# Performance work log

Measured on AMD Instinct MI355X. Metric: run time of the kernel, lower is better.

## Reference

```python
import jax, jax.numpy as jnp
import numpy as np

BIT = 4
HALF = 2 ** (BIT - 1)          # 8 -> signed integer grid [-8, 7]
N_LEVELS = 2 ** BIT - 1        # 15
COUT, CIN, KH, KW = 1024, 1024, 3, 3


def _flip_pass(r, err, up_num, up_err, up_pri, dn_num, dn_err, dn_pri):
    """One SQuant flip pass over rows (groups). Greedily flips the rounding
    direction of the highest-priority elements so each row's rounding-error
    sum becomes ~0, and hands off boundary priorities for the next pass
    (reconstruction of the SQuant_func CUDA kernel)."""
    G, K = r.shape
    rows = jnp.arange(G)
    e = err.sum(-1)                                    # (G,) error budget
    nflip = jnp.round(jnp.abs(e)).astype(jnp.int32)    # flips needed per row
    is_up = e < 0                                      # under-rounded -> flip up

    pri = jnp.where(is_up[:, None], up_pri, dn_pri)
    order = jnp.argsort(-pri, axis=-1)                 # descending priority
    rank = jnp.zeros((G, K), jnp.int32).at[rows[:, None], order].set(
        jnp.broadcast_to(jnp.arange(K, dtype=jnp.int32), (G, K)))
    flip = rank < nflip[:, None]

    cand_num = jnp.where(is_up[:, None], up_num, dn_num)
    cand_err = jnp.where(is_up[:, None], up_err, dn_err)
    new_r = jnp.where(flip, cand_num, r)
    new_err = jnp.where(flip, cand_err, err)

    # ---- boundary-priority handoff for the next (channel-wise) pass ----
    ni = jnp.take_along_axis(order, jnp.clip(nflip, 0, K - 1)[:, None], axis=-1)[:, 0]      # next candidate
    li = jnp.take_along_axis(order, jnp.clip(nflip - 1, 0, K - 1)[:, None], axis=-1)[:, 0]  # last flipped
    has_next = nflip < K
    has_last = nflip > 0
    next_pri = jnp.where(has_next, pri[rows, ni], 0.0)         # flip one more element
    last_pri = jnp.where(has_last, 1.0 - pri[rows, li], 0.0)   # revert the last flip

    z = jnp.zeros_like(pri)
    new_up_pri = z.at[rows, ni].add(jnp.where(is_up, next_pri, 0.0))
    new_up_pri = new_up_pri.at[rows, li].add(jnp.where(~is_up, last_pri, 0.0))
    new_dn_pri = z.at[rows, ni].add(jnp.where(~is_up, next_pri, 0.0))
    new_dn_pri = new_dn_pri.at[rows, li].add(jnp.where(is_up, last_pri, 0.0))

    # reverting the last flipped element restores its pre-flip value/error
    up_last = is_up & has_last
    dn_last = (~is_up) & has_last
    new_dn_num = dn_num.at[rows, li].set(jnp.where(up_last, r[rows, li], dn_num[rows, li]))
    new_dn_err = dn_err.at[rows, li].set(jnp.where(up_last, err[rows, li], dn_err[rows, li]))
    new_up_num = up_num.at[rows, li].set(jnp.where(dn_last, r[rows, li], up_num[rows, li]))
    new_up_err = up_err.at[rows, li].set(jnp.where(dn_last, err[rows, li], up_err[rows, li]))
    return new_r, new_err, new_up_num, new_up_err, new_up_pri, new_dn_num, new_dn_err, new_dn_pri


def _adaptive_round(q):
    t_min, t_max = float(-HALF), float(HALF - 1)
    r = jnp.round(q)
    err = r - q
    cand_up = (err < 0) & (q < t_max)    # elements that may be rounded up instead
    cand_dn = (err > 0) & (q > t_min)    # elements that may be rounded down instead
    up_num = jnp.where(cand_up, r + 1.0, r)
    up_err = jnp.where(cand_up, err + 1.0, 0.0)
    up_pri = jnp.where(cand_up, -err, 0.0)   # |rounding error|
    dn_num = jnp.where(cand_dn, r - 1.0, r)
    dn_err = jnp.where(cand_dn, err - 1.0, 0.0)
    dn_pri = jnp.where(cand_dn, err, 0.0)

    cout, cin = q.shape[0], q.shape[1]
    k = q.size // (cout * cin)
    st = tuple(a.reshape(cout * cin, k) for a in (r, err, up_num, up_err, up_pri, dn_num, dn_err, dn_pri))
    st = _flip_pass(*st)                               # SQuant-K: per (Cout,Cin) kernel
    st = tuple(a.reshape(cout, cin * k) for a in st)
    st = _flip_pass(*st)                               # SQuant-C: per output channel
    return st[0].reshape(q.shape)


def _squant_quantize(weight):
    flat = weight.reshape(weight.shape[0], -1)
    x_max = flat.max(1)
    x_min = flat.min(1)
    scale = N_LEVELS / jnp.maximum(x_max - x_min, 1e-8)   # asymmetric per-channel
    zp = jnp.round(scale * x_min) + HALF                  # signed, integral zero point
    bshape = (-1,) + (1,) * (weight.ndim - 1)
    scale = scale.reshape(bshape)
    zp = zp.reshape(bshape)
    q = scale * weight - zp                               # linear_quantize
    q = _adaptive_round(q)
    q = jnp.clip(q, -HALF, HALF - 1)
    return (q + zp) / scale                               # linear_dequantize


def setup_inputs() -> dict:
    key = jax.random.key(0)
    weight = jax.random.normal(key, (COUT, CIN, KH, KW), dtype=jnp.float32) * 0.05
    return {"weight": weight}


def reference(weight):
    return _squant_quantize(weight)
```

## Files before the change

### kernel.cpp

```cpp
#include <hip/hip_runtime.h>

#define NROW   1024
#define ROWLEN 9216
#define NGRP   1024
#define NT     256
#define GPT    4
#define LCAP   256

__device__ __forceinline__ int bucketOf(float v) {
    int b = (int)(v * 256.0f);
    return b > 255 ? 255 : b;
}

__device__ __forceinline__ float err2_of(float wv, int enc, float scale, float zp) {
    float q = __fsub_rn(__fmul_rn(scale, wv), zp);
    float r = rintf(q);
    float err = __fsub_rn(r, q);
    if (enc > 50) return 0.0f;
    int delta = enc - __float2int_rn(r);
    return delta ? __fadd_rn(err, (float)delta) : err;
}

__device__ void replay_group(const float* wg, float scale, float zp,
                             float r[9], float err[9], float q[9],
                             int* nflip1, bool* isup1, int* li_out) {
    float pri[9];
    #pragma unroll
    for (int j = 0; j < 9; ++j) {
        float qq = __fsub_rn(__fmul_rn(scale, wg[j]), zp);
        float rr = rintf(qq);
        q[j] = qq; r[j] = rr; err[j] = __fsub_rn(rr, qq);
    }
    float e = __fadd_rn(
                __fadd_rn(__fadd_rn(__fadd_rn(err[0], err[1]), __fadd_rn(err[2], err[3])),
                          __fadd_rn(__fadd_rn(err[4], err[5]), __fadd_rn(err[6], err[7]))),
                err[8]);
    int nf0 = (int)rintf(fabsf(e));
    bool up = (e < 0.0f);
    #pragma unroll
    for (int j = 0; j < 9; ++j) {
        bool cand = up ? ((err[j] < 0.0f) && (q[j] < 7.0f))
                       : ((err[j] > 0.0f) && (q[j] > -8.0f));
        pri[j] = cand ? (up ? -err[j] : err[j]) : 0.0f;
    }
    int rank[9] = {0,0,0,0,0,0,0,0,0};
    #pragma unroll
    for (int a = 0; a < 9; ++a)
        #pragma unroll
        for (int b = a + 1; b < 9; ++b) {
            int c = (pri[a] >= pri[b]) ? 1 : 0;
            rank[b] += c; rank[a] += 1 - c;
        }
    int nf = nf0 < 9 ? nf0 : 9;
    int lip = nf - 1; if (lip < 0) lip = 0;
    int li = 0;
    #pragma unroll
    for (int j = 0; j < 9; ++j) if (rank[j] == lip) li = j;
    *nflip1 = nf0; *isup1 = up; *li_out = li;
}

__global__ __launch_bounds__(NT, 5) void squant_kernel(const float* __restrict__ w,
                                                       float* __restrict__ out) {
    __shared__ alignas(16) signed char s_r2[ROWLEN];
    __shared__ unsigned short s_upos[NGRP];
    __shared__ unsigned short s_dpos[NGRP];
    __shared__ float s_uval[NGRP];
    __shared__ float s_dval[NGRP];
    __shared__ signed char s_ucn[NGRP];
    __shared__ signed char s_dcn[NGRP];
    __shared__ float s_leaf[128];
    __shared__ int   s_hist[256];
    __shared__ float s_lv[LCAP];
    __shared__ unsigned short s_lg[LCAP];
    __shared__ float s_wred[8];
    __shared__ float s_bc[2];
    __shared__ float s_e2s;
    __shared__ int   s_seli[2];
    __shared__ int   s_lcount;

    const int row = blockIdx.x;
    const int tid = threadIdx.x;
    const int lane = tid & 63, wid = tid >> 6;
    const float* wrow = w + (size_t)row * ROWLEN;

    float vmin =  3.402823466e38f;
    float vmax = -3.402823466e38f;
    const float4* w4 = reinterpret_cast<const float4*>(wrow);
    #pragma unroll
    for (int k = 0; k < 9; ++k) {
        float4 v = w4[tid + k * NT];
        vmin = fminf(vmin, fminf(fminf(v.x, v.y), fminf(v.z, v.w)));
        vmax = fmaxf(vmax, fmaxf(fmaxf(v.x, v.y), fmaxf(v.z, v.w)));
    }
    #pragma unroll
    for (int o = 32; o > 0; o >>= 1) {
        vmin = fminf(vmin, __shfl_xor(vmin, o, 64));
        vmax = fmaxf(vmax, __shfl_xor(vmax, o, 64));
    }
    if (lane == 0) { s_wred[wid] = vmin; s_wred[4 + wid] = vmax; }
    __syncthreads();
    if (tid == 0) {
        float a = s_wred[0], b = s_wred[4];
        #pragma unroll
        for (int i = 1; i < 4; ++i) { a = fminf(a, s_wred[i]); b = fmaxf(b, s_wred[4 + i]); }
        s_bc[0] = a; s_bc[1] = b;
    }
    __syncthreads();
    const float scale = __fdiv_rn(15.0f, fmaxf(__fsub_rn(s_bc[1], s_bc[0]), 1e-8f));
    const float zp    = __fadd_rn(rintf(__fmul_rn(scale, s_bc[0])), 8.0f);

    const float4* wt4 = reinterpret_cast<const float4*>(wrow + 36 * tid);
    #pragma unroll
    for (int gi = 0; gi < GPT; ++gi) {
        const int g = tid * GPT + gi;
        const int base = g * 9;
        const int a4 = (9 * gi) >> 2;
        float4 A = wt4[a4], B = wt4[a4 + 1], C = wt4[a4 + 2];
        float f[12] = {A.x, A.y, A.z, A.w, B.x, B.y, B.z, B.w, C.x, C.y, C.z, C.w};
        float q[9], r[9], err[9], pri[9];
        #pragma unroll
        for (int j = 0; j < 9; ++j) {
            float wv = f[gi + j];
            float qq = __fsub_rn(__fmul_rn(scale, wv), zp);
            float rr = rintf(qq);
            q[j] = qq; r[j] = rr; err[j] = __fsub_rn(rr, qq);
        }
        float e = __fadd_rn(
                    __fadd_rn(__fadd_rn(__fadd_rn(err[0], err[1]), __fadd_rn(err[2], err[3])),
                              __fadd_rn(__fadd_rn(err[4], err[5]), __fadd_rn(err[6], err[7]))),
                    err[8]);
        int nflip = (int)rintf(fabsf(e));
        const bool isup = (e < 0.0f);
        #pragma unroll
        for (int j = 0; j < 9; ++j) {
            bool cand = isup ? ((err[j] < 0.0f) && (q[j] < 7.0f))
                             : ((err[j] > 0.0f) && (q[j] > -8.0f));
            pri[j] = cand ? (isup ? -err[j] : err[j]) : 0.0f;
        }
        int rank[9] = {0,0,0,0,0,0,0,0,0};
        #pragma unroll
        for (int a = 0; a < 9; ++a)
            #pragma unroll
            for (int b = a + 1; b < 9; ++b) {
                int c = (pri[a] >= pri[b]) ? 1 : 0;
                rank[b] += c; rank[a] += 1 - c;
            }
        const int nf  = nflip < 9 ? nflip : 9;
        const int nip = nf < 8 ? nf : 8;
        int lip = nf - 1; if (lip < 0) lip = 0;

        int ni = 0, li = 0;
        float pri_ni = 0.0f, pri_li = 0.0f, r_ni = 0.0f, r_li = 0.0f;
        #pragma unroll
        for (int j = 0; j < 9; ++j) {
            bool cand = pri[j] > 0.0f;
            bool flip = rank[j] < nf;
            float cnj = cand ? (isup ? r[j] + 1.0f : r[j] - 1.0f) : r[j];
            int enc = __float2int_rn(flip ? cnj : r[j]);
            if (flip && !cand) enc += 100;
            s_r2[base + j] = (signed char)enc;
            if (rank[j] == nip) { ni = j; pri_ni = pri[j]; r_ni = r[j]; }
            if (rank[j] == lip) { li = j; pri_li = pri[j]; r_li = r[j]; }
        }
        const bool has_next = (nflip < 9);
        const bool has_last = (nflip > 0);
        const float next_pri = has_next ? pri_ni : 0.0f;
        const float last_pri = has_last ? __fsub_rn(1.0f, pri_li) : 0.0f;
        signed char ncv = (signed char)__float2int_rn(
            (pri_ni > 0.0f) ? (isup ? r_ni + 1.0f : r_ni - 1.0f) : r_ni);
        signed char lcv = (signed char)__float2int_rn(r_li);
        if (isup) {
            s_upos[g] = (unsigned short)(base + ni); s_uval[g] = next_pri; s_ucn[g] = ncv;
            s_dpos[g] = (unsigned short)(base + li); s_dval[g] = last_pri; s_dcn[g] = lcv;
        } else {
            s_dpos[g] = (unsigned short)(base + ni); s_dval[g] = next_pri; s_dcn[g] = ncv;
            s_upos[g] = (unsigned short)(base + li); s_uval[g] = last_pri; s_ucn[g] = lcv;
        }
    }
    __syncthreads();

    {
        const int l = tid >> 1, h = tid & 1;
        float a0, a1, a2, a3;
        #pragma unroll
        for (int i = 0; i < 9; ++i) {
            const int off = 72 * l + 8 * i + 4 * h;
            float4 v = *reinterpret_cast<const float4*>(wrow + off);
            int e4 = *reinterpret_cast<const int*>(s_r2 + off);
            float e0 = err2_of(v.x, (int)(signed char)(e4 & 0xff),         scale, zp);
            float e1 = err2_of(v.y, (int)(signed char)((e4 >> 8) & 0xff),  scale, zp);
            float e2v= err2_of(v.z, (int)(signed char)((e4 >> 16) & 0xff), scale, zp);
            float e3 = err2_of(v.w, (int)(signed char)((e4 >> 24) & 0xff), scale, zp);
            if (i == 0) { a0 = e0; a1 = e1; a2 = e2v; a3 = e3; }
            else {
                a0 = __fadd_rn(a0, e0); a1 = __fadd_rn(a1, e1);
                a2 = __fadd_rn(a2, e2v); a3 = __fadd_rn(a3, e3);
            }
        }
        float t = __fadd_rn(__fadd_rn(a0, a1), __fadd_rn(a2, a3));
        float o = __shfl_xor(t, 1, 64);
        if (h == 0) s_leaf[l] = __fadd_rn(t, o);
        s_hist[tid] = 0;
        if (tid == 0) s_lcount = 0;
    }
    __syncthreads();
    if (tid < 64) {
        float v = __fadd_rn(s_leaf[2 * tid], s_leaf[2 * tid + 1]);
        #pragma unroll
        for (int o = 1; o < 64; o <<= 1) {
            float u = __shfl_xor(v, o, 64);
            v = __fadd_rn(v, u);
        }
        if (tid == 0) s_e2s = v;
    }
    __syncthreads();

    const float e2     = s_e2s;
    const int   nflip2 = (int)rintf(fabsf(e2));
    const bool  isup2  = (e2 < 0.0f);
    const float* val = isup2 ? s_uval : s_dval;
    const unsigned short* pos = isup2 ? s_upos : s_dpos;
    const signed char* cnv = isup2 ? s_ucn : s_dcn;

    int   gg[4]; float vv[4]; int bb[4];
    #pragma unroll
    for (int m = 0; m < 4; ++m) {
        gg[m] = tid + m * NT;
        vv[m] = val[gg[m]];
        bb[m] = (vv[m] > 0.0f) ? bucketOf(vv[m]) : -1;
        if (bb[m] >= 0) atomicAdd(&s_hist[bb[m]], 1);
    }
    __syncthreads();
    if (tid < 64) {
        int b0 = s_hist[4*tid], b1 = s_hist[4*tid+1], b2 = s_hist[4*tid+2], b3 = s_hist[4*tid+3];
        int s3 = b3, s2 = b2 + s3, s1 = b1 + s2, s0 = b0 + s1;
        int suf = s0;
        #pragma unroll
        for (int off = 1; off < 64; off <<= 1) {
            int o = __shfl_down(suf, off, 64);
            if (tid + off < 64) suf += o;
        }
        int above = suf - s0;
        s_hist[4*tid]   = s0 + above;
        s_hist[4*tid+1] = s1 + above;
        s_hist[4*tid+2] = s2 + above;
        s_hist[4*tid+3] = s3 + above;
    }
    __syncthreads();
    const int npos = s_hist[0];

    if (nflip2 > 0 && nflip2 <= npos) {
        {
            int Tb  = s_hist[tid];
            int Tb1 = (tid < 255) ? s_hist[tid + 1] : 0;
            if (Tb >= nflip2 && Tb1 < nflip2) { s_seli[0] = tid; s_seli[1] = nflip2 - Tb1; }
        }
        __syncthreads();
        const int B = s_seli[0], m = s_seli[1];
        #pragma unroll
        for (int mm = 0; mm < 4; ++mm) {
            if (bb[mm] > B) s_r2[pos[gg[mm]]] = cnv[gg[mm]];
            else if (bb[mm] == B) {
                int ix = atomicAdd(&s_lcount, 1);
                if (ix < LCAP) { s_lv[ix] = vv[mm]; s_lg[ix] = (unsigned short)gg[mm]; }
            }
        }
        __syncthreads();
        const int L = s_lcount;
        if (L <= LCAP) {
            #pragma unroll
            for (int mm = 0; mm < 4; ++mm) {
                if (bb[mm] != B) continue;
                int rk = 0;
                for (int l = 0; l < L; ++l) {
                    float lv = s_lv[l]; int lg = s_lg[l];
                    rk += (int)((lv > vv[mm]) || ((lv == vv[mm]) && (lg < gg[mm])));
                }
                if (rk < m) s_r2[pos[gg[mm]]] = cnv[gg[mm]];
            }
        } else {
            #pragma unroll
            for (int mm = 0; mm < 4; ++mm) {
                if (bb[mm] != B) continue;
                int rk = 0;
                for (int j = 0; j < NGRP; ++j) {
                    float vj = val[j];
                    if (vj > 0.0f && bucketOf(vj) == B)
                        rk += (int)((vj > vv[mm]) || ((vj == vv[mm]) && (j < gg[mm])));
                }
                if (rk < m) s_r2[pos[gg[mm]]] = cnv[gg[mm]];
            }
        }
    } else if (nflip2 > npos) {
        #pragma unroll
        for (int mm = 0; mm < 4; ++mm)
            if (bb[mm] >= 0) s_r2[pos[gg[mm]]] = cnv[gg[mm]];
        __syncthreads();
        if (tid == 0) {
            int c = 0; const int extra = nflip2 - npos;
            for (int g = 0; g < NGRP && c < extra; ++g) {
                float r[9], err[9], q[9]; int nf1; bool up1; int li;
                replay_group(wrow + 9 * g, scale, zp, r, err, q, &nf1, &up1, &li);
                for (int j = 0; j < 9 && c < extra; ++j) {
                    int p = 9 * g + j;
                    if (val[g] > 0.0f && pos[g] == p) continue;
                    float cnp;
                    if (isup2) { bool cu = (err[j] < 0.0f) && (q[j] < 7.0f);
                                 cnp = cu ? r[j] + 1.0f : r[j]; }
                    else       { bool cd = (err[j] > 0.0f) && (q[j] > -8.0f);
                                 cnp = cd ? r[j] - 1.0f : r[j]; }
                    if (nf1 > 0 && j == li && (up1 != isup2)) cnp = r[j];
                    s_r2[p] = (signed char)__float2int_rn(cnp);
                    ++c;
                }
            }
        }
    }
    __syncthreads();

    const int* r2i = reinterpret_cast<const int*>(s_r2);
    float4* o4 = reinterpret_cast<float4*>(out + (size_t)row * ROWLEN);
    #pragma unroll
    for (int k = 0; k < 9; ++k) {
        int i = tid + k * NT;
        int word = r2i[i];
        float4 o;
        #pragma unroll
        for (int c = 0; c < 4; ++c) {
            int v = (int)(signed char)((word >> (8 * c)) & 0xff);
            if (v > 50) v -= 100;
            v = v < -8 ? -8 : (v > 7 ? 7 : v);
            float f = __fdiv_rn(__fadd_rn((float)v, zp), scale);
            if (c == 0) o.x = f; else if (c == 1) o.y = f; else if (c == 2) o.z = f; else o.w = f;
        }
        o4[i] = o;
    }
}

extern "C" void kernel_launch(void* const* d_in, const int* in_sizes, int n_in,
                              void* d_out, int out_size, void* d_ws, size_t ws_size,
                              hipStream_t stream) {
    const float* w = (const float*)d_in[0];
    float* out = (float*)d_out;
    squant_kernel<<<dim3(NROW), dim3(NT), 0, stream>>>(w, out);
}
```

Before: 109.3 us.

## Keep row weights and pass-1 errors in registers to skip reload and recompute

```diff
diff --git a/kernel.cpp b/kernel.cpp
--- a/kernel.cpp
+++ b/kernel.cpp
@@ -12,15 +12,6 @@
     return b > 255 ? 255 : b;
 }
 
-__device__ __forceinline__ float err2_of(float wv, int enc, float scale, float zp) {
-    float q = __fsub_rn(__fmul_rn(scale, wv), zp);
-    float r = rintf(q);
-    float err = __fsub_rn(r, q);
-    if (enc > 50) return 0.0f;
-    int delta = enc - __float2int_rn(r);
-    return delta ? __fadd_rn(err, (float)delta) : err;
-}
-
 __device__ void replay_group(const float* wg, float scale, float zp,
                              float r[9], float err[9], float q[9],
                              int* nflip1, bool* isup1, int* li_out) {
@@ -59,7 +50,7 @@
     *nflip1 = nf0; *isup1 = up; *li_out = li;
 }
 
-__global__ __launch_bounds__(NT, 5) void squant_kernel(const float* __restrict__ w,
+__global__ __launch_bounds__(NT, 4) void squant_kernel(const float* __restrict__ w,
                                                        float* __restrict__ out) {
     __shared__ alignas(16) signed char s_r2[ROWLEN];
     __shared__ unsigned short s_upos[NGRP];
@@ -83,12 +74,14 @@
     const int lane = tid & 63, wid = tid >> 6;
     const float* wrow = w + (size_t)row * ROWLEN;
 
+    float fe[36];
     float vmin =  3.402823466e38f;
     float vmax = -3.402823466e38f;
-    const float4* w4 = reinterpret_cast<const float4*>(wrow);
+    const float4* wt4 = reinterpret_cast<const float4*>(wrow + 36 * tid);
     #pragma unroll
     for (int k = 0; k < 9; ++k) {
-        float4 v = w4[tid + k * NT];
+        float4 v = wt4[k];
+        fe[4*k+0] = v.x; fe[4*k+1] = v.y; fe[4*k+2] = v.z; fe[4*k+3] = v.w;
         vmin = fminf(vmin, fminf(fminf(v.x, v.y), fminf(v.z, v.w)));
         vmax = fmaxf(vmax, fmaxf(fmaxf(v.x, v.y), fmaxf(v.z, v.w)));
     }
@@ -109,18 +102,15 @@
     const float scale = __fdiv_rn(15.0f, fmaxf(__fsub_rn(s_bc[1], s_bc[0]), 1e-8f));
     const float zp    = __fadd_rn(rintf(__fmul_rn(scale, s_bc[0])), 8.0f);
 
-    const float4* wt4 = reinterpret_cast<const float4*>(wrow + 36 * tid);
+    int pk[9] = {0,0,0,0,0,0,0,0,0};
     #pragma unroll
     for (int gi = 0; gi < GPT; ++gi) {
         const int g = tid * GPT + gi;
         const int base = g * 9;
-        const int a4 = (9 * gi) >> 2;
-        float4 A = wt4[a4], B = wt4[a4 + 1], C = wt4[a4 + 2];
-        float f[12] = {A.x, A.y, A.z, A.w, B.x, B.y, B.z, B.w, C.x, C.y, C.z, C.w};
         float q[9], r[9], err[9], pri[9];
         #pragma unroll
         for (int j = 0; j < 9; ++j) {
-            float wv = f[gi + j];
+            float wv = fe[9 * gi + j];
             float qq = __fsub_rn(__fmul_rn(scale, wv), zp);
             float rr = rintf(qq);
             q[j] = qq; r[j] = rr; err[j] = __fsub_rn(rr, qq);
@@ -156,9 +146,11 @@
             bool cand = pri[j] > 0.0f;
             bool flip = rank[j] < nf;
             float cnj = cand ? (isup ? r[j] + 1.0f : r[j] - 1.0f) : r[j];
-            int enc = __float2int_rn(flip ? cnj : r[j]);
-            if (flip && !cand) enc += 100;
-            s_r2[base + j] = (signed char)enc;
+            float cej = cand ? (isup ? __fadd_rn(err[j], 1.0f) : __fsub_rn(err[j], 1.0f)) : 0.0f;
+            fe[9 * gi + j] = flip ? cej : err[j];
+            int enc = __float2int_rn(flip ? cnj : r[j]) & 0xff;
+            const int m = 9 * gi + j;
+            pk[m >> 2] |= enc << (8 * (m & 3));
             if (rank[j] == nip) { ni = j; pri_ni = pri[j]; r_ni = r[j]; }
             if (rank[j] == lip) { li = j; pri_li = pri[j]; r_li = r[j]; }
         }
@@ -177,29 +169,35 @@
             s_upos[g] = (unsigned short)(base + li); s_uval[g] = last_pri; s_ucn[g] = lcv;
         }
     }
-    __syncthreads();
-
     {
-        const int l = tid >> 1, h = tid & 1;
-        float a0, a1, a2, a3;
-        #pragma unroll
-        for (int i = 0; i < 9; ++i) {
-            const int off = 72 * l + 8 * i + 4 * h;
-            float4 v = *reinterpret_cast<const float4*>(wrow + off);
-            int e4 = *reinterpret_cast<const int*>(s_r2 + off);
-            float e0 = err2_of(v.x, (int)(signed char)(e4 & 0xff),         scale, zp);
-            float e1 = err2_of(v.y, (int)(signed char)((e4 >> 8) & 0xff),  scale, zp);
-            float e2v= err2_of(v.z, (int)(signed char)((e4 >> 16) & 0xff), scale, zp);
-            float e3 = err2_of(v.w, (int)(signed char)((e4 >> 24) & 0xff), scale, zp);
-            if (i == 0) { a0 = e0; a1 = e1; a2 = e2v; a3 = e3; }
-            else {
-                a0 = __fadd_rn(a0, e0); a1 = __fadd_rn(a1, e1);
-                a2 = __fadd_rn(a2, e2v); a3 = __fadd_rn(a3, e3);
-            }
-        }
-        float t = __fadd_rn(__fadd_rn(a0, a1), __fadd_rn(a2, a3));
-        float o = __shfl_xor(t, 1, 64);
-        if (h == 0) s_leaf[l] = __fadd_rn(t, o);
+        int* r2w = reinterpret_cast<int*>(s_r2);
+        #pragma unroll
+        for (int k = 0; k < 9; ++k) r2w[9 * tid + k] = pk[k];
+    }
+
+    {
+        const int h = tid & 1;
+        float pe[8];
+        #pragma unroll
+        for (int j = 0; j < 8; ++j) {
+            float s = __fadd_rn(__fadd_rn(__fadd_rn(fe[j], fe[8 + j]), fe[16 + j]), fe[24 + j]);
+            if (j < 4) s = __fadd_rn(s, fe[32 + j]);
+            pe[j] = s;
+        }
+        #pragma unroll
+        for (int j = 0; j < 8; ++j) pe[j] = __shfl_xor(pe[j], 1, 64);
+        float po[8];
+        #pragma unroll
+        for (int j = 0; j < 4; ++j)
+            po[j] = __fadd_rn(__fadd_rn(__fadd_rn(__fadd_rn(pe[j], fe[4 + j]),
+                                                  fe[12 + j]), fe[20 + j]), fe[28 + j]);
+        #pragma unroll
+        for (int j = 4; j < 8; ++j)
+            po[j] = __fadd_rn(__fadd_rn(__fadd_rn(__fadd_rn(__fadd_rn(pe[j], fe[j - 4]),
+                                                  fe[4 + j]), fe[12 + j]), fe[20 + j]), fe[28 + j]);
+        float res = __fadd_rn(__fadd_rn(__fadd_rn(po[0], po[1]), __fadd_rn(po[2], po[3])),
+                              __fadd_rn(__fadd_rn(po[4], po[5]), __fadd_rn(po[6], po[7])));
+        if (h) s_leaf[tid >> 1] = res;
         s_hist[tid] = 0;
         if (tid == 0) s_lcount = 0;
     }
@@ -328,7 +326,6 @@
         #pragma unroll
         for (int c = 0; c < 4; ++c) {
             int v = (int)(signed char)((word >> (8 * c)) & 0xff);
-            if (v > 50) v -= 100;
             v = v < -8 ? -8 : (v > 7 ? 7 : v);
             float f = __fdiv_rn(__fadd_rn((float)v, zp), scale);
             if (c == 0) o.x = f; else if (c == 1) o.y = f; else if (c == 2) o.z = f; else o.w = f;
```

New measurement: 136.3 us. 24.8% more time.
